# Optimization experiments

Hardware: AMD Instinct MI355X
Metric: run time of the kernel (lower is better)

Reference implementation:

```python
import jax, jax.numpy as jnp
import numpy as np

B, C, H, W = 8, 512, 64, 64
CH = C // 2          # channels per branch after chunk
R = CH // 4          # reduced channels (reduction=4)


def conv1x1(x, w, b):
    # x: [B,c,H,W], w: [o,c], b: [o]  (1x1 conv == per-pixel matmul)
    return jnp.einsum('oc,bchw->bohw', w, x) + b[None, :, None, None]


def spatial_self_corr(x, w1, b1, w2, b2, wo, bo):
    # DANet-style position attention. x: [B,CH,H,W]
    b_, c_, h_, w_ = x.shape
    n = h_ * w_
    q = conv1x1(x, w1, b1).reshape(b_, -1, n)   # [B,R,N]
    k = conv1x1(x, w2, b2).reshape(b_, -1, n)   # [B,R,N]
    attn = jax.nn.softmax(jnp.einsum('brn,brm->bnm', q, k), axis=-1)  # [B,N,N]
    out = jnp.einsum('brn,bnm->brm', k, attn)   # v = k (reduced channels), [B,R,N]
    out = out.reshape(b_, -1, h_, w_)
    return conv1x1(out, wo, bo)                 # [B,CH,H,W]


def channel_self_corr(x, wq, bq, wk, bk, wo, bo):
    # DANet-style channel attention over reduced channels. x: [B,CH,H,W]
    b_, c_, h_, w_ = x.shape
    n = h_ * w_
    q = conv1x1(x, wq, bq).reshape(b_, -1, n)   # [B,R,N]
    k = conv1x1(x, wk, bk).reshape(b_, -1, n)   # [B,R,N]
    attn = jax.nn.softmax(jnp.einsum('brn,bsn->brs', q, k), axis=-1)  # [B,R,R]
    out = jnp.einsum('brs,bsn->brn', attn, k)   # v = k (reduced channels)
    out = out.reshape(b_, -1, h_, w_)
    return conv1x1(out, wo, bo)                 # [B,CH,H,W]


def ckam_forward(top_feat, bottom_feat, wt, bt, wb, bb,
                 s_w1, s_b1, s_w2, s_b2, s_wo, s_bo,
                 c_wq, c_bq, c_wk, c_bk, c_wo, c_bo, f_w, f_b):
    top = conv1x1(top_feat, wt, bt)
    bottom = conv1x1(bottom_feat, wb, bb)
    x = top + bottom                            # [B,C,H,W]
    x1, x2 = jnp.split(x, 2, axis=1)            # each [B,C/2,H,W]
    ssc_out = spatial_self_corr(x1, s_w1, s_b1, s_w2, s_b2, s_wo, s_bo)
    csc_out = channel_self_corr(x2, c_wq, c_bq, c_wk, c_bk, c_wo, c_bo)
    out = jnp.concatenate([ssc_out, csc_out], axis=1)  # [B,C,H,W]
    return conv1x1(out, f_w, f_b)


def setup_inputs() -> dict:
    key = jax.random.key(0)
    ks = jax.random.split(key, 24)
    s = 0.02
    d = {
        'top_feat': jax.random.normal(ks[0], (B, C, H, W), jnp.float32),
        'bottom_feat': jax.random.normal(ks[1], (B, C, H, W), jnp.float32),
        'wt': jax.random.normal(ks[2], (C, C), jnp.float32) * s,
        'bt': jnp.zeros((C,), jnp.float32),
        'wb': jax.random.normal(ks[3], (C, C), jnp.float32) * s,
        'bb': jnp.zeros((C,), jnp.float32),
        's_w1': jax.random.normal(ks[4], (R, CH), jnp.float32) * s,
        's_b1': jnp.zeros((R,), jnp.float32),
        's_w2': jax.random.normal(ks[5], (R, CH), jnp.float32) * s,
        's_b2': jnp.zeros((R,), jnp.float32),
        's_wo': jax.random.normal(ks[6], (CH, R), jnp.float32) * s,
        's_bo': jnp.zeros((CH,), jnp.float32),
        'c_wq': jax.random.normal(ks[7], (R, CH), jnp.float32) * s,
        'c_bq': jnp.zeros((R,), jnp.float32),
        'c_wk': jax.random.normal(ks[8], (R, CH), jnp.float32) * s,
        'c_bk': jnp.zeros((R,), jnp.float32),
        'c_wo': jax.random.normal(ks[9], (CH, R), jnp.float32) * s,
        'c_bo': jnp.zeros((CH,), jnp.float32),
        'f_w': jax.random.normal(ks[10], (C, C), jnp.float32) * s,
        'f_b': jnp.zeros((C,), jnp.float32),
    }
    return d


def reference(top_feat, bottom_feat, wt, bt, wb, bb,
              s_w1, s_b1, s_w2, s_b2, s_wo, s_bo,
              c_wq, c_bq, c_wk, c_bk, c_wo, c_bo, f_w, f_b):
    return ckam_forward(top_feat, bottom_feat, wt, bt, wb, bb,
                        s_w1, s_b1, s_w2, s_b2, s_wo, s_bo,
                        c_wq, c_bq, c_wk, c_bk, c_wo, c_bo, f_w, f_b)
```

## Files before the change

kernel.cpp:

```cpp
#include <hip/hip_runtime.h>

typedef unsigned short u16;
typedef unsigned int   u32;
typedef __attribute__((ext_vector_type(8))) short short8;
typedef __attribute__((ext_vector_type(4))) float f32x4;

__device__ __forceinline__ u16 f2bf(float f) {
  u32 u = __float_as_uint(f);
  u32 r = u + 0x7fffu + ((u >> 16) & 1u);
  return (u16)(r >> 16);
}

__device__ __forceinline__ void gl_lds16(const u16* g, u16* l) {
  __builtin_amdgcn_global_load_lds(
      (const __attribute__((address_space(1))) u32*)g,
      (__attribute__((address_space(3))) u32*)l, 16, 0, 0);
}

__global__ __launch_bounds__(256) void k_combine_qk(
    const float* __restrict__ wt, const float* __restrict__ bt,
    const float* __restrict__ wb, const float* __restrict__ bb,
    const float* __restrict__ s_w1, const float* __restrict__ s_b1,
    const float* __restrict__ s_w2, const float* __restrict__ s_b2,
    const float* __restrict__ c_wq, const float* __restrict__ c_bq,
    const float* __restrict__ c_wk, const float* __restrict__ c_bk,
    u16* __restrict__ Wqkb, float* __restrict__ bqk) {
  int j = blockIdx.x;
  int g = j >> 6, r = j & 63;
  const float* sw; const float* sb;
  if (g == 0)      { sw = s_w1; sb = s_b1; }
  else if (g == 1) { sw = s_w2; sb = s_b2; }
  else if (g == 2) { sw = c_wq; sb = c_bq; }
  else             { sw = c_wk; sb = c_bk; }
  int cbase = (g < 2) ? 0 : 256;

  __shared__ float swr[256];
  __shared__ float red[256];
  int t = threadIdx.x;
  swr[t] = sw[r * 256 + t];
  __syncthreads();

  float a0 = 0.f, a1 = 0.f, a2 = 0.f, a3 = 0.f;
#pragma unroll 4
  for (int c = 0; c < 256; ++c) {
    float a = swr[c];
    int row = (cbase + c) * 512;
    a0 += a * wt[row + t];
    a1 += a * wt[row + 256 + t];
    a2 += a * wb[row + t];
    a3 += a * wb[row + 256 + t];
  }
  Wqkb[j * 1024 + t]       = f2bf(a0);
  Wqkb[j * 1024 + 256 + t] = f2bf(a1);
  Wqkb[j * 1024 + 512 + t] = f2bf(a2);
  Wqkb[j * 1024 + 768 + t] = f2bf(a3);

  red[t] = swr[t] * (bt[cbase + t] + bb[cbase + t]);
  __syncthreads();
  for (int s = 128; s > 0; s >>= 1) {
    if (t < s) red[t] += red[t + s];
    __syncthreads();
  }
  if (t == 0) bqk[j] = red[0] + sb[r];
}

__global__ __launch_bounds__(128) void k_combine_f(
    const float* __restrict__ f_w, const float* __restrict__ f_b,
    const float* __restrict__ s_wo, const float* __restrict__ s_bo,
    const float* __restrict__ c_wo, const float* __restrict__ c_bo,
    u16* __restrict__ Wfb, float* __restrict__ bfb) {
  int o = blockIdx.x;
  int t = threadIdx.x;
  __shared__ float fwr[512];
  __shared__ float red[128];
  for (int i = t; i < 512; i += 128) fwr[i] = f_w[o * 512 + i];
  __syncthreads();

  float acc = 0.f;
  if (t < 64) {
#pragma unroll 4
    for (int c = 0; c < 256; ++c) acc += fwr[c] * s_wo[c * 64 + t];
  } else {
    int rr = t - 64;
#pragma unroll 4
    for (int c = 0; c < 256; ++c) acc += fwr[256 + c] * c_wo[c * 64 + rr];
  }
  Wfb[o * 128 + t] = f2bf(acc);

  red[t] = fwr[t] * s_bo[t] + fwr[t + 128] * s_bo[t + 128]
         + fwr[256 + t] * c_bo[t] + fwr[384 + t] * c_bo[t + 128];
  __syncthreads();
  for (int s = 64; s > 0; s >>= 1) {
    if (t < s) red[t] += red[t + s];
    __syncthreads();
  }
  if (t == 0) bfb[o] = red[0] + f_b[o];
}

__global__ __launch_bounds__(256) void k_gemm_qk_mfma(
    const float* __restrict__ top, const float* __restrict__ bot,
    const u16* __restrict__ Wqkb, const float* __restrict__ bqk,
    float* __restrict__ qk) {
  int b = blockIdx.z, j0 = blockIdx.y * 128, n0 = blockIdx.x * 128;
  __shared__ __align__(16) u16 Aj[2][128][32];
  __shared__ __align__(16) u16 Xs[2][128][32];
  int t = threadIdx.x;
  int wv = t >> 6, lane = t & 63;
  int wr = wv >> 1, wc = wv & 1;
  int q = lane >> 4, l = lane & 15;

  f32x4 acc[4][4];
#pragma unroll
  for (int tr = 0; tr < 4; ++tr)
#pragma unroll
    for (int tc = 0; tc < 4; ++tc) acc[tr][tc] = (f32x4){0.f, 0.f, 0.f, 0.f};

  int xn = t & 31;
  int xs = t >> 5;
  int kx = (xn + (xn >> 2)) & 3;
  int wcol = ((((xs >> 1) ^ kx) << 4) | ((xs & 1) << 3));
  int asr4 = lane >> 2;
  int asc = (lane & 3) ^ ((asr4 + (asr4 >> 2)) & 3);
  int rowA = wr * 64 + l;
  int rowX = wc * 64 + l;
  int fswA = (q ^ ((rowA + (rowA >> 2)) & 3)) << 4;
  int fswX = (q ^ ((rowX + (rowX >> 2)) & 3)) << 4;

  float xva[16], xvb[16];

  auto stageA = [&](int kc, u16* dst) {
#pragma unroll
    for (int pp = 0; pp < 2; ++pp) {
      int p = wv * 2 + pp;
      int row = p * 16 + asr4;
      gl_lds16(Wqkb + (size_t)(j0 + row) * 1024 + kc + asc * 8, dst + p * 512);
    }
  };
  auto loadX = [&](int kc, float (&xv)[16]) {
    const float* src = (kc < 512) ? top : bot;
    int c0 = kc & 511;
    const float* xb = src + (size_t)(b * 512 + c0) * 4096 + n0;
#pragma unroll
    for (int p = 0; p < 4; ++p) {
      int n = xn + 32 * p;
#pragma unroll
      for (int d = 0; d < 4; ++d)
        xv[4 * p + d] = xb[(size_t)(4 * xs + d) * 4096 + n];
    }
  };
  auto writeX = [&](float (&xv)[16], u16* dst) {
    char* base = reinterpret_cast<char*>(dst);
#pragma unroll
    for (int p = 0; p < 4; ++p) {
      int n = xn + 32 * p;
      uint2 pk;
      pk.x = (u32)f2bf(xv[4 * p])     | ((u32)f2bf(xv[4 * p + 1]) << 16);
      pk.y = (u32)f2bf(xv[4 * p + 2]) | ((u32)f2bf(xv[4 * p + 3]) << 16);
      *reinterpret_cast<uint2*>(base + n * 64 + wcol) = pk;
    }
  };
  auto compute = [&](int bufsel) {
    const char* Ab = reinterpret_cast<const char*>(&Aj[bufsel][0][0]);
    const char* Xb = reinterpret_cast<const char*>(&Xs[bufsel][0][0]);
    short8 af[4], bfr[4];
#pragma unroll
    for (int tr = 0; tr < 4; ++tr)
      af[tr] = *reinterpret_cast<const short8*>(Ab + (rowA + tr * 16) * 64 + fswA);
#pragma unroll
    for (int tc = 0; tc < 4; ++tc)
      bfr[tc] = *reinterpret_cast<const short8*>(Xb + (rowX + tc * 16) * 64 + fswX);
#pragma unroll
    for (int tr = 0; tr < 4; ++tr)
#pragma unroll
      for (int tc = 0; tc < 4; ++tc)
        acc[tr][tc] = __builtin_amdgcn_mfma_f32_16x16x32_bf16(
            af[tr], bfr[tc], acc[tr][tc], 0, 0, 0);
  };

  stageA(0, &Aj[0][0][0]);
  loadX(0, xva);
  writeX(xva, &Xs[0][0][0]);
  loadX(32, xvb);
  asm volatile("s_waitcnt lgkmcnt(0)" ::: "memory");
  __builtin_amdgcn_s_barrier();

  for (int it2 = 0; it2 < 15; ++it2) {
    int e = it2 * 2;
    stageA((e + 1) * 32, &Aj[1][0][0]);
    loadX((e + 2) * 32, xva);
    writeX(xvb, &Xs[1][0][0]);
    compute(0);
    asm volatile("s_waitcnt vmcnt(16) lgkmcnt(0)" ::: "memory");
    __builtin_amdgcn_s_barrier();
    stageA((e + 2) * 32, &Aj[0][0][0]);
    loadX((e + 3) * 32, xvb);
    writeX(xva, &Xs[0][0][0]);
    compute(1);
    asm volatile("s_waitcnt vmcnt(16) lgkmcnt(0)" ::: "memory");
    __builtin_amdgcn_s_barrier();
  }
  stageA(31 * 32, &Aj[1][0][0]);
  writeX(xvb, &Xs[1][0][0]);
  compute(0);
  asm volatile("s_waitcnt vmcnt(0) lgkmcnt(0)" ::: "memory");
  __builtin_amdgcn_s_barrier();
  compute(1);

#pragma unroll
  for (int tr = 0; tr < 4; ++tr) {
    int j = j0 + wr * 64 + tr * 16 + q * 4;
    float4 bias = *reinterpret_cast<const float4*>(&bqk[j]);
#pragma unroll
    for (int tc = 0; tc < 4; ++tc) {
      int n = n0 + wc * 64 + tc * 16 + l;
      float* dst = qk + (size_t)(b * 256 + j) * 4096 + n;
      dst[0]        = acc[tr][tc][0] + bias.x;
      dst[4096]     = acc[tr][tc][1] + bias.y;
      dst[2 * 4096] = acc[tr][tc][2] + bias.z;
      dst[3 * 4096] = acc[tr][tc][3] + bias.w;
    }
  }
}

__global__ __launch_bounds__(256) void k_transpose_qk(
    const float* __restrict__ qk, u16* __restrict__ q1t, u16* __restrict__ k1t) {
  int b = blockIdx.y, n0 = blockIdx.x * 64;
  __shared__ u16 T[128][68];
  int t = threadIdx.x;
  for (int i = t; i < 8192; i += 256) {
    int j = i >> 6, n = i & 63;
    T[j][n] = f2bf(qk[((size_t)(b * 256) + j) * 4096 + n0 + n]);
  }
  __syncthreads();
  int n = t & 63, h = t >> 6;
  u16 buf[32];
#pragma unroll
  for (int jj = 0; jj < 32; ++jj) buf[jj] = T[h * 32 + jj][n];
  u16* dst;
  if (h < 2) dst = q1t + ((size_t)(b * 4096) + n0 + n) * 64 + h * 32;
  else       dst = k1t + ((size_t)(b * 4096) + n0 + n) * 64 + (h - 2) * 32;
  u32* d32 = reinterpret_cast<u32*>(dst);
#pragma unroll
  for (int k = 0; k < 16; ++k)
    d32[k] = (u32)buf[2 * k] | ((u32)buf[2 * k + 1] << 16);
}

__global__ __launch_bounds__(256) void k_sp_stats_mfma(
    const u16* __restrict__ q1t, const u16* __restrict__ k1t,
    const float* __restrict__ qk, u16* __restrict__ k1d) {
  int b = blockIdx.y, n0 = blockIdx.x * 64;
  __shared__ u16 Qs[64][72];
  __shared__ float red[4][64][16];
  __shared__ float dvs[64];
  int t = threadIdx.x;
  int wv = t >> 6, lane = t & 63;
  int q = lane >> 4, l = lane & 15;

  {
    const u32* src = reinterpret_cast<const u32*>(q1t + ((size_t)(b * 4096) + n0) * 64);
    for (int i = t; i < 2048; i += 256) {
      int n = i >> 5, c = i & 31;
      reinterpret_cast<u32*>(&Qs[n][0])[c] = src[n * 32 + c];
    }
  }
  __syncthreads();

  short8 afr[4][2];
#pragma unroll
  for (int tn = 0; tn < 4; ++tn)
#pragma unroll
    for (int kh = 0; kh < 2; ++kh)
      afr[tn][kh] = *reinterpret_cast<const short8*>(&Qs[tn * 16 + l][kh * 32 + q * 8]);

  const u16* kbase = k1t + (size_t)b * 4096 * 64;
  float dsum[4][4];
#pragma unroll
  for (int tn = 0; tn < 4; ++tn)
#pragma unroll
    for (int i = 0; i < 4; ++i) dsum[tn][i] = 0.f;

  for (int mt = wv; mt < 64; mt += 4) {
    int m0 = mt * 64;
#pragma unroll
    for (int tm = 0; tm < 4; ++tm) {
      const u16* kp = kbase + ((size_t)(m0 + tm * 16 + l)) * 64;
      short8 b0 = *reinterpret_cast<const short8*>(kp + q * 8);
      short8 b1 = *reinterpret_cast<const short8*>(kp + 32 + q * 8);
#pragma unroll
      for (int tn = 0; tn < 4; ++tn) {
        f32x4 acc = {0.f, 0.f, 0.f, 0.f};
        acc = __builtin_amdgcn_mfma_f32_16x16x32_bf16(afr[tn][0], b0, acc, 0, 0, 0);
        acc = __builtin_amdgcn_mfma_f32_16x16x32_bf16(afr[tn][1], b1, acc, 0, 0, 0);
#pragma unroll
        for (int i = 0; i < 4; ++i) dsum[tn][i] += __expf(acc[i]);
      }
    }
  }

#pragma unroll
  for (int tn = 0; tn < 4; ++tn)
#pragma unroll
    for (int i = 0; i < 4; ++i)
      red[wv][tn * 16 + q * 4 + i][l] = dsum[tn][i];
  __syncthreads();
  if (t < 64) {
    float s = 0.f;
#pragma unroll
    for (int v = 0; v < 4; ++v)
#pragma unroll
      for (int u = 0; u < 16; ++u) s += red[v][t][u];
    dvs[t] = 1.0f / s;
  }
  __syncthreads();

  const float* k1src = qk + ((size_t)(b * 256) + 64) * 4096 + n0;
  u16* kdst = k1d + (size_t)(b * 64) * 4096 + n0;
  for (int i = t; i < 4096; i += 256) {
    int r = i >> 6, n = i & 63;
    kdst[(size_t)r * 4096 + n] = f2bf(k1src[(size_t)r * 4096 + n] * dvs[n]);
  }
}

#define NSPLIT 2

__device__ __forceinline__ void stage_qk(const u16* qb, const u16* kb, int noff,
                                         u16* qdst, u16* kdst,
                                         int wv, int rsub, int scol) {
#pragma unroll
  for (int pp = 0; pp < 2; ++pp) {
    int p = wv * 2 + pp;
    int row = p * 8 + rsub;
    gl_lds16(qb + ((size_t)(noff + row)) * 64 + scol * 8, qdst + p * 512);
    gl_lds16(kb + (size_t)row * 4096 + noff + scol * 8, kdst + p * 512);
  }
}

__global__ __launch_bounds__(256) void k_sp_apply_mfma(
    const u16* __restrict__ q1t, const u16* __restrict__ k1t,
    const u16* __restrict__ k1d, float* __restrict__ spre) {
  int b = blockIdx.z, m0 = blockIdx.x * 64;
  int n_base = blockIdx.y * (4096 / NSPLIT);
  const int NT = 64 / NSPLIT;

  __shared__ __align__(16) u16 Qs[2][64][64];
  __shared__ __align__(16) u16 Ks[2][64][64];
  __shared__ __align__(16) u16 Wt[64][64];

  int t = threadIdx.x;
  int wv = t >> 6, lane = t & 63;
  int q = lane >> 4, l = lane & 15;
  int sw = l & 7;
  int rsub = lane >> 3;
  int scol = (lane & 7) ^ rsub;

  const u16* ktp = k1t + ((size_t)(b * 4096) + m0 + wv * 16 + l) * 64;
  short8 bS0 = *reinterpret_cast<const short8*>(ktp + q * 8);
  short8 bS1 = *reinterpret_cast<const short8*>(ktp + 32 + q * 8);

  const u16* qb = q1t + (size_t)b * 4096 * 64;
  const u16* kb = k1d + (size_t)b * 64 * 4096;

  f32x4 accO[4];
#pragma unroll
  for (int tr = 0; tr < 4; ++tr) accO[tr] = (f32x4){0.f, 0.f, 0.f, 0.f};

  stage_qk(qb, kb, n_base, &Qs[0][0][0], &Ks[0][0][0], wv, rsub, scol);
  __syncthreads();

  int wrow = wv * 16 + l;
  char* wp = reinterpret_cast<char*>(&Wt[wrow][0]);
  int c_a0 = (q ^ sw) << 4;
  int c_a1 = c_a0 ^ 64;

  int cur = 0;
  for (int nt = 0; nt < NT; ++nt) {
    if (nt + 1 < NT)
      stage_qk(qb, kb, n_base + (nt + 1) * 64,
               &Qs[cur ^ 1][0][0], &Ks[cur ^ 1][0][0], wv, rsub, scol);

    const u16(*Qc)[64] = Qs[cur];
    const u16(*Kc)[64] = Ks[cur];

#pragma unroll
    for (int tn = 0; tn < 4; ++tn) {
      const char* qrow = reinterpret_cast<const char*>(&Qc[tn * 16 + l][0]);
      short8 a0 = *reinterpret_cast<const short8*>(qrow + c_a0);
      short8 a1 = *reinterpret_cast<const short8*>(qrow + c_a1);
      f32x4 s = {0.f, 0.f, 0.f, 0.f};
      s = __builtin_amdgcn_mfma_f32_16x16x32_bf16(a0, bS0, s, 0, 0, 0);
      s = __builtin_amdgcn_mfma_f32_16x16x32_bf16(a1, bS1, s, 0, 0, 0);
      u16 w0 = f2bf(__expf(s[0]));
      u16 w1 = f2bf(__expf(s[1]));
      u16 w2 = f2bf(__expf(s[2]));
      u16 w3 = f2bf(__expf(s[3]));
      uint2 pk;
      pk.x = (u32)w0 | ((u32)w1 << 16);
      pk.y = (u32)w2 | ((u32)w3 << 16);
      *reinterpret_cast<uint2*>(
          wp + ((((tn * 2 + (q >> 1)) ^ sw) << 4) | ((q & 1) << 3))) = pk;
    }

    short8 bW0 = *reinterpret_cast<const short8*>(wp + c_a0);
    short8 bW1 = *reinterpret_cast<const short8*>(wp + c_a1);
#pragma unroll
    for (int tr = 0; tr < 4; ++tr) {
      const char* krow = reinterpret_cast<const char*>(&Kc[tr * 16 + l][0]);
      short8 a0 = *reinterpret_cast<const short8*>(krow + c_a0);
      short8 a1 = *reinterpret_cast<const short8*>(krow + c_a1);
      accO[tr] = __builtin_amdgcn_mfma_f32_16x16x32_bf16(a0, bW0, accO[tr], 0, 0, 0);
      accO[tr] = __builtin_amdgcn_mfma_f32_16x16x32_bf16(a1, bW1, accO[tr], 0, 0, 0);
    }

    __syncthreads();
    cur ^= 1;
  }

#pragma unroll
  for (int tr = 0; tr < 4; ++tr)
#pragma unroll
    for (int i = 0; i < 4; ++i)
      atomicAdd(&spre[(size_t)(b * 64 + tr * 16 + q * 4 + i) * 4096 + m0 + wrow],
                accO[tr][i]);
}

__global__ __launch_bounds__(256) void k_ch_scores(
    const float* __restrict__ qk, float* __restrict__ part) {
  int b = blockIdx.y, ch = blockIdx.x;
  const float* q2 = qk + (size_t)(b * 256 + 128) * 4096;
  const float* k2 = qk + (size_t)(b * 256 + 192) * 4096;
  __shared__ float Qs[64][65];
  __shared__ float Ks[64][65];
  int t = threadIdx.x, ti = t >> 4, tj = t & 15;
  float acc[4][4] = {};

  for (int sub = 0; sub < 2; ++sub) {
    int n0 = ch * 128 + sub * 64;
    __syncthreads();
    for (int i = t; i < 4096; i += 256) {
      int r = i >> 6, n = i & 63;
      Qs[r][n] = q2[(size_t)r * 4096 + n0 + n];
      Ks[r][n] = k2[(size_t)r * 4096 + n0 + n];
    }
    __syncthreads();
#pragma unroll
    for (int n = 0; n < 64; ++n) {
      float qa[4], ka[4];
#pragma unroll
      for (int i = 0; i < 4; ++i) qa[i] = Qs[ti * 4 + i][n];
#pragma unroll
      for (int jx = 0; jx < 4; ++jx) ka[jx] = Ks[tj * 4 + jx][n];
#pragma unroll
      for (int i = 0; i < 4; ++i)
#pragma unroll
        for (int jx = 0; jx < 4; ++jx) acc[i][jx] += qa[i] * ka[jx];
    }
  }
#pragma unroll
  for (int i = 0; i < 4; ++i)
#pragma unroll
    for (int jx = 0; jx < 4; ++jx)
      part[(size_t)(b * 32 + ch) * 4096 + (ti * 4 + i) * 64 + tj * 4 + jx] = acc[i][jx];
}

__global__ __launch_bounds__(64) void k_ch_softmax(
    const float* __restrict__ part, float* __restrict__ attn2) {
  int bid = blockIdx.x;
  int b = bid >> 6, r = bid & 63;
  int s = threadIdx.x;
  const float* p0 = part + (size_t)(b * 32) * 4096 + r * 64 + s;
  float sum = 0.f;
#pragma unroll
  for (int c = 0; c < 32; ++c) sum += p0[(size_t)c * 4096];
  float mx = sum;
#pragma unroll
  for (int o = 32; o > 0; o >>= 1) mx = fmaxf(mx, __shfl_xor(mx, o));
  float e = __expf(sum - mx);
  float den = e;
#pragma unroll
  for (int o = 32; o > 0; o >>= 1) den += __shfl_xor(den, o);
  attn2[(size_t)b * 4096 + r * 64 + s] = e / den;
}

__global__ __launch_bounds__(256) void k_ch_apply(
    const float* __restrict__ qk, const float* __restrict__ attn2,
    float* __restrict__ cpre) {
  int b = blockIdx.y;
  int t = threadIdx.x;
  int n = blockIdx.x * 64 + (t & 63);
  int qr = t >> 6;
  const float* k2 = qk + (size_t)(b * 256 + 192) * 4096;
  __shared__ float As[64][64];
  {
    float4* As4 = reinterpret_cast<float4*>(&As[0][0]);
    const float4* a4 = reinterpret_cast<const float4*>(attn2 + (size_t)b * 4096);
    for (int i = t; i < 1024; i += 256) As4[i] = a4[i];
  }
  __syncthreads();

  float acc[16];
#pragma unroll
  for (int rr = 0; rr < 16; ++rr) acc[rr] = 0.f;
  for (int s4 = 0; s4 < 64; s4 += 4) {
    float kv0 = k2[(size_t)(s4 + 0) * 4096 + n];
    float kv1 = k2[(size_t)(s4 + 1) * 4096 + n];
    float kv2 = k2[(size_t)(s4 + 2) * 4096 + n];
    float kv3 = k2[(size_t)(s4 + 3) * 4096 + n];
#pragma unroll
    for (int rr = 0; rr < 16; ++rr) {
      float4 w = *reinterpret_cast<const float4*>(&As[qr * 16 + rr][s4]);
      acc[rr] += w.x * kv0 + w.y * kv1 + w.z * kv2 + w.w * kv3;
    }
  }
#pragma unroll
  for (int rr = 0; rr < 16; ++rr)
    cpre[(size_t)(b * 64 + qr * 16 + rr) * 4096 + n] = acc[rr];
}

__global__ __launch_bounds__(256) void k_final_mfma(
    const float* __restrict__ spre, const float* __restrict__ cpre,
    const u16* __restrict__ Wfb, const float* __restrict__ bfb,
    float* __restrict__ out) {
  int b = blockIdx.z, o0 = blockIdx.y * 128, n0 = blockIdx.x * 128;
  __shared__ u16 Aj[128][40];
  __shared__ u16 Xs[128][40];
  int t = threadIdx.x;
  int wv = t >> 6, lane = t & 63;
  int wr = wv >> 1, wc = wv & 1;
  int q = lane >> 4, l = lane & 15;

  f32x4 acc[4][4];
#pragma unroll
  for (int tr = 0; tr < 4; ++tr)
#pragma unroll
    for (int tc = 0; tc < 4; ++tc) acc[tr][tc] = (f32x4){0.f, 0.f, 0.f, 0.f};

  int xn = t & 31;
  int xs = t >> 5;

  for (int kc = 0; kc < 128; kc += 32) {
    __syncthreads();
    {
      const u32* asrc = reinterpret_cast<const u32*>(Wfb + (size_t)o0 * 128 + kc);
#pragma unroll
      for (int p = 0; p < 8; ++p) {
        int i = p * 256 + t;
        int row = i >> 4, c = i & 15;
        *reinterpret_cast<u32*>(&Aj[row][c * 2]) = asrc[(size_t)row * 64 + c];
      }
    }
    const float* src = (kc < 64) ? spre : cpre;
    int r0 = (kc < 64) ? kc : kc - 64;
    const float* xb = src + (size_t)(b * 64 + r0) * 4096 + n0;
#pragma unroll
    for (int p = 0; p < 8; ++p) {
      int n = xn + 32 * (p >> 1);
      int kp = xs + 8 * (p & 1);
      float v0 = xb[(size_t)(2 * kp) * 4096 + n];
      float v1 = xb[(size_t)(2 * kp + 1) * 4096 + n];
      *reinterpret_cast<u32*>(&Xs[n][kp * 2]) =
          (u32)f2bf(v0) | ((u32)f2bf(v1) << 16);
    }
    __syncthreads();

    short8 af[4], bfr[4];
#pragma unroll
    for (int tr = 0; tr < 4; ++tr)
      af[tr] = *reinterpret_cast<const short8*>(&Aj[wr * 64 + tr * 16 + l][q * 8]);
#pragma unroll
    for (int tc = 0; tc < 4; ++tc)
      bfr[tc] = *reinterpret_cast<const short8*>(&Xs[wc * 64 + tc * 16 + l][q * 8]);
#pragma unroll
    for (int tr = 0; tr < 4; ++tr)
#pragma unroll
      for (int tc = 0; tc < 4; ++tc)
        acc[tr][tc] = __builtin_amdgcn_mfma_f32_16x16x32_bf16(
            af[tr], bfr[tc], acc[tr][tc], 0, 0, 0);
  }

#pragma unroll
  for (int tr = 0; tr < 4; ++tr) {
    int o = o0 + wr * 64 + tr * 16 + q * 4;
    float4 bias = *reinterpret_cast<const float4*>(&bfb[o]);
#pragma unroll
    for (int tc = 0; tc < 4; ++tc) {
      int n = n0 + wc * 64 + tc * 16 + l;
      float* dst = out + (size_t)(b * 512 + o) * 4096 + n;
      dst[0]        = acc[tr][tc][0] + bias.x;
      dst[4096]     = acc[tr][tc][1] + bias.y;
      dst[2 * 4096] = acc[tr][tc][2] + bias.z;
      dst[3 * 4096] = acc[tr][tc][3] + bias.w;
    }
  }
}

extern "C" void kernel_launch(void* const* d_in, const int* in_sizes, int n_in,
                              void* d_out, int out_size, void* d_ws, size_t ws_size,
                              hipStream_t stream) {
  const float* top  = (const float*)d_in[0];
  const float* bot  = (const float*)d_in[1];
  const float* wt   = (const float*)d_in[2];
  const float* bt   = (const float*)d_in[3];
  const float* wb   = (const float*)d_in[4];
  const float* bb   = (const float*)d_in[5];
  const float* s_w1 = (const float*)d_in[6];
  const float* s_b1 = (const float*)d_in[7];
  const float* s_w2 = (const float*)d_in[8];
  const float* s_b2 = (const float*)d_in[9];
  const float* s_wo = (const float*)d_in[10];
  const float* s_bo = (const float*)d_in[11];
  const float* c_wq = (const float*)d_in[12];
  const float* c_bq = (const float*)d_in[13];
  const float* c_wk = (const float*)d_in[14];
  const float* c_bk = (const float*)d_in[15];
  const float* c_wo = (const float*)d_in[16];
  const float* c_bo = (const float*)d_in[17];
  const float* f_w  = (const float*)d_in[18];
  const float* f_b  = (const float*)d_in[19];
  float* out = (float*)d_out;

  char* ob = (char*)d_out;
  float* qk = (float*)ob;
  u16* q1t = (u16*)(ob + 33554432);
  u16* k1t = (u16*)(ob + 37748736);
  u16* k1d = (u16*)(ob + 41943040);
  float* part = (float*)(ob + 46137344);

  char* ws = (char*)d_ws;
  float* attn2 = (float*)(ws + 1179648);
  float* spre  = (float*)(ws + 1310720);
  float* cpre  = (float*)(ws + 9699328);
  u16*   Wqkb  = (u16*)  (ws + 18087936);
  float* bqk   = (float*)(ws + 18612224);
  u16*   Wfb   = (u16*)  (ws + 18613248);
  float* bfb   = (float*)(ws + 18744320);

  hipMemsetAsync(spre, 0, 8388608, stream);

  k_combine_qk<<<256, 256, 0, stream>>>(wt, bt, wb, bb, s_w1, s_b1, s_w2, s_b2,
                                        c_wq, c_bq, c_wk, c_bk, Wqkb, bqk);
  k_combine_f<<<512, 128, 0, stream>>>(f_w, f_b, s_wo, s_bo, c_wo, c_bo, Wfb, bfb);
  k_gemm_qk_mfma<<<dim3(32, 2, 8), 256, 0, stream>>>(top, bot, Wqkb, bqk, qk);
  k_transpose_qk<<<dim3(64, 8), 256, 0, stream>>>(qk, q1t, k1t);
  k_sp_stats_mfma<<<dim3(64, 8), 256, 0, stream>>>(q1t, k1t, qk, k1d);
  k_ch_scores<<<dim3(32, 8), 256, 0, stream>>>(qk, part);
  k_ch_softmax<<<512, 64, 0, stream>>>(part, attn2);
  k_ch_apply<<<dim3(64, 8), 256, 0, stream>>>(qk, attn2, cpre);
  k_sp_apply_mfma<<<dim3(64, NSPLIT, 8), 256, 0, stream>>>(q1t, k1t, k1d, spre);
  k_final_mfma<<<dim3(32, 4, 8), 256, 0, stream>>>(spre, cpre, Wfb, bfb, out);
}
```

Baseline: 433.2 us.

## Vectorize fp32 activation loads and double-buffer the final GEMM

The QK projection GEMM now loads activations as float4 vectors, with each thread covering four adjacent pixels, and the vmcnt waits are adjusted to match the smaller number of load instructions. The transpose kernel drops its LDS staging and reads float4 rows directly, packing bf16 into 16-byte stores. The final 1x1 GEMM is rebuilt on the same double-buffered, swizzled LDS pipeline, with async global-to-LDS weight staging. The aim is fewer memory instructions and better overlap of loads with MFMA work. The risk is that the uint2 LDS writes may hit more bank conflicts.

```diff
diff --git a/kernel.cpp b/kernel.cpp
--- a/kernel.cpp
+++ b/kernel.cpp
@@ -115,10 +115,8 @@
 #pragma unroll
     for (int tc = 0; tc < 4; ++tc) acc[tr][tc] = (f32x4){0.f, 0.f, 0.f, 0.f};
 
-  int xn = t & 31;
+  int a = t & 31;
   int xs = t >> 5;
-  int kx = (xn + (xn >> 2)) & 3;
-  int wcol = ((((xs >> 1) ^ kx) << 4) | ((xs & 1) << 3));
   int asr4 = lane >> 2;
   int asc = (lane & 3) ^ ((asr4 + (asr4 >> 2)) & 3);
   int rowA = wr * 64 + l;
@@ -126,7 +124,7 @@
   int fswA = (q ^ ((rowA + (rowA >> 2)) & 3)) << 4;
   int fswX = (q ^ ((rowX + (rowX >> 2)) & 3)) << 4;
 
-  float xva[16], xvb[16];
+  f32x4 xva[4], xvb[4];
 
   auto stageA = [&](int kc, u16* dst) {
 #pragma unroll
@@ -136,27 +134,25 @@
       gl_lds16(Wqkb + (size_t)(j0 + row) * 1024 + kc + asc * 8, dst + p * 512);
     }
   };
-  auto loadX = [&](int kc, float (&xv)[16]) {
+  auto loadX = [&](int kc, f32x4 (&xv)[4]) {
     const float* src = (kc < 512) ? top : bot;
     int c0 = kc & 511;
-    const float* xb = src + (size_t)(b * 512 + c0) * 4096 + n0;
-#pragma unroll
-    for (int p = 0; p < 4; ++p) {
-      int n = xn + 32 * p;
-#pragma unroll
-      for (int d = 0; d < 4; ++d)
-        xv[4 * p + d] = xb[(size_t)(4 * xs + d) * 4096 + n];
-    }
-  };
-  auto writeX = [&](float (&xv)[16], u16* dst) {
+    const float* xb = src + (size_t)(b * 512 + c0) * 4096 + n0 + 4 * a;
+#pragma unroll
+    for (int d = 0; d < 4; ++d)
+      xv[d] = *reinterpret_cast<const f32x4*>(&xb[(size_t)(4 * xs + d) * 4096]);
+  };
+  auto writeX = [&](f32x4 (&xv)[4], u16* dst) {
     char* base = reinterpret_cast<char*>(dst);
 #pragma unroll
-    for (int p = 0; p < 4; ++p) {
-      int n = xn + 32 * p;
+    for (int i = 0; i < 4; ++i) {
+      int n = 4 * a + i;
+      int key = (n + (n >> 2)) & 3;
+      int col = ((((xs >> 1) ^ key) << 4) | ((xs & 1) << 3));
       uint2 pk;
-      pk.x = (u32)f2bf(xv[4 * p])     | ((u32)f2bf(xv[4 * p + 1]) << 16);
-      pk.y = (u32)f2bf(xv[4 * p + 2]) | ((u32)f2bf(xv[4 * p + 3]) << 16);
-      *reinterpret_cast<uint2*>(base + n * 64 + wcol) = pk;
+      pk.x = (u32)f2bf(xv[0][i]) | ((u32)f2bf(xv[1][i]) << 16);
+      pk.y = (u32)f2bf(xv[2][i]) | ((u32)f2bf(xv[3][i]) << 16);
+      *reinterpret_cast<uint2*>(base + n * 64 + col) = pk;
     }
   };
   auto compute = [&](int bufsel) {
@@ -190,13 +186,13 @@
     loadX((e + 2) * 32, xva);
     writeX(xvb, &Xs[1][0][0]);
     compute(0);
-    asm volatile("s_waitcnt vmcnt(16) lgkmcnt(0)" ::: "memory");
+    asm volatile("s_waitcnt vmcnt(4) lgkmcnt(0)" ::: "memory");
     __builtin_amdgcn_s_barrier();
     stageA((e + 2) * 32, &Aj[0][0][0]);
     loadX((e + 3) * 32, xvb);
     writeX(xva, &Xs[0][0][0]);
     compute(1);
-    asm volatile("s_waitcnt vmcnt(16) lgkmcnt(0)" ::: "memory");
+    asm volatile("s_waitcnt vmcnt(4) lgkmcnt(0)" ::: "memory");
     __builtin_amdgcn_s_barrier();
   }
   stageA(31 * 32, &Aj[1][0][0]);
@@ -225,24 +221,27 @@
 __global__ __launch_bounds__(256) void k_transpose_qk(
     const float* __restrict__ qk, u16* __restrict__ q1t, u16* __restrict__ k1t) {
   int b = blockIdx.y, n0 = blockIdx.x * 64;
-  __shared__ u16 T[128][68];
-  int t = threadIdx.x;
-  for (int i = t; i < 8192; i += 256) {
-    int j = i >> 6, n = i & 63;
-    T[j][n] = f2bf(qk[((size_t)(b * 256) + j) * 4096 + n0 + n]);
-  }
-  __syncthreads();
-  int n = t & 63, h = t >> 6;
-  u16 buf[32];
-#pragma unroll
-  for (int jj = 0; jj < 32; ++jj) buf[jj] = T[h * 32 + jj][n];
-  u16* dst;
-  if (h < 2) dst = q1t + ((size_t)(b * 4096) + n0 + n) * 64 + h * 32;
-  else       dst = k1t + ((size_t)(b * 4096) + n0 + n) * 64 + (h - 2) * 32;
-  u32* d32 = reinterpret_cast<u32*>(dst);
-#pragma unroll
-  for (int k = 0; k < 16; ++k)
-    d32[k] = (u32)buf[2 * k] | ((u32)buf[2 * k + 1] << 16);
+  int t = threadIdx.x;
+  int a = t & 15;
+  int c = t >> 4;
+  int jb = 8 * (c & 7);
+  const float* src =
+      qk + ((size_t)(b * 256) + (c >> 3) * 64 + jb) * 4096 + n0 + 4 * a;
+  f32x4 v[8];
+#pragma unroll
+  for (int i = 0; i < 8; ++i)
+    v[i] = *reinterpret_cast<const f32x4*>(&src[(size_t)i * 4096]);
+  u16* dstbase = (c < 8) ? q1t : k1t;
+#pragma unroll
+  for (int i = 0; i < 4; ++i) {
+    int n = n0 + 4 * a + i;
+    u32 pk[4];
+#pragma unroll
+    for (int kk = 0; kk < 4; ++kk)
+      pk[kk] = (u32)f2bf(v[2 * kk][i]) | ((u32)f2bf(v[2 * kk + 1][i]) << 16);
+    *reinterpret_cast<uint4*>(dstbase + ((size_t)(b * 4096) + n) * 64 + jb) =
+        *reinterpret_cast<const uint4*>(pk);
+  }
 }
 
 __global__ __launch_bounds__(256) void k_sp_stats_mfma(
@@ -521,8 +520,8 @@
     const u16* __restrict__ Wfb, const float* __restrict__ bfb,
     float* __restrict__ out) {
   int b = blockIdx.z, o0 = blockIdx.y * 128, n0 = blockIdx.x * 128;
-  __shared__ u16 Aj[128][40];
-  __shared__ u16 Xs[128][40];
+  __shared__ __align__(16) u16 Aj[2][128][32];
+  __shared__ __align__(16) u16 Xs[2][128][32];
   int t = threadIdx.x;
   int wv = t >> 6, lane = t & 63;
   int wr = wv >> 1, wc = wv & 1;
@@ -534,48 +533,88 @@
 #pragma unroll
     for (int tc = 0; tc < 4; ++tc) acc[tr][tc] = (f32x4){0.f, 0.f, 0.f, 0.f};
 
-  int xn = t & 31;
+  int a = t & 31;
   int xs = t >> 5;
-
-  for (int kc = 0; kc < 128; kc += 32) {
-    __syncthreads();
-    {
-      const u32* asrc = reinterpret_cast<const u32*>(Wfb + (size_t)o0 * 128 + kc);
-#pragma unroll
-      for (int p = 0; p < 8; ++p) {
-        int i = p * 256 + t;
-        int row = i >> 4, c = i & 15;
-        *reinterpret_cast<u32*>(&Aj[row][c * 2]) = asrc[(size_t)row * 64 + c];
-      }
-    }
+  int asr4 = lane >> 2;
+  int asc = (lane & 3) ^ ((asr4 + (asr4 >> 2)) & 3);
+  int rowA = wr * 64 + l;
+  int rowX = wc * 64 + l;
+  int fswA = (q ^ ((rowA + (rowA >> 2)) & 3)) << 4;
+  int fswX = (q ^ ((rowX + (rowX >> 2)) & 3)) << 4;
+
+  f32x4 xva[4], xvb[4];
+
+  auto stageA = [&](int kc, u16* dst) {
+#pragma unroll
+    for (int pp = 0; pp < 2; ++pp) {
+      int p = wv * 2 + pp;
+      int row = p * 16 + asr4;
+      gl_lds16(Wfb + (size_t)(o0 + row) * 128 + kc + asc * 8, dst + p * 512);
+    }
+  };
+  auto loadX = [&](int kc, f32x4 (&xv)[4]) {
     const float* src = (kc < 64) ? spre : cpre;
-    int r0 = (kc < 64) ? kc : kc - 64;
-    const float* xb = src + (size_t)(b * 64 + r0) * 4096 + n0;
-#pragma unroll
-    for (int p = 0; p < 8; ++p) {
-      int n = xn + 32 * (p >> 1);
-      int kp = xs + 8 * (p & 1);
-      float v0 = xb[(size_t)(2 * kp) * 4096 + n];
-      float v1 = xb[(size_t)(2 * kp + 1) * 4096 + n];
-      *reinterpret_cast<u32*>(&Xs[n][kp * 2]) =
-          (u32)f2bf(v0) | ((u32)f2bf(v1) << 16);
-    }
-    __syncthreads();
-
+    int r0 = kc & 63;
+    const float* xb = src + (size_t)(b * 64 + r0) * 4096 + n0 + 4 * a;
+#pragma unroll
+    for (int d = 0; d < 4; ++d)
+      xv[d] = *reinterpret_cast<const f32x4*>(&xb[(size_t)(4 * xs + d) * 4096]);
+  };
+  auto writeX = [&](f32x4 (&xv)[4], u16* dst) {
+    char* base = reinterpret_cast<char*>(dst);
+#pragma unroll
+    for (int i = 0; i < 4; ++i) {
+      int n = 4 * a + i;
+      int key = (n + (n >> 2)) & 3;
+      int col = ((((xs >> 1) ^ key) << 4) | ((xs & 1) << 3));
+      uint2 pk;
+      pk.x = (u32)f2bf(xv[0][i]) | ((u32)f2bf(xv[1][i]) << 16);
+      pk.y = (u32)f2bf(xv[2][i]) | ((u32)f2bf(xv[3][i]) << 16);
+      *reinterpret_cast<uint2*>(base + n * 64 + col) = pk;
+    }
+  };
+  auto compute = [&](int bufsel) {
+    const char* Ab = reinterpret_cast<const char*>(&Aj[bufsel][0][0]);
+    const char* Xb = reinterpret_cast<const char*>(&Xs[bufsel][0][0]);
     short8 af[4], bfr[4];
 #pragma unroll
     for (int tr = 0; tr < 4; ++tr)
-      af[tr] = *reinterpret_cast<const short8*>(&Aj[wr * 64 + tr * 16 + l][q * 8]);
+      af[tr] = *reinterpret_cast<const short8*>(Ab + (rowA + tr * 16) * 64 + fswA);
 #pragma unroll
     for (int tc = 0; tc < 4; ++tc)
-      bfr[tc] = *reinterpret_cast<const short8*>(&Xs[wc * 64 + tc * 16 + l][q * 8]);
+      bfr[tc] = *reinterpret_cast<const short8*>(Xb + (rowX + tc * 16) * 64 + fswX);
 #pragma unroll
     for (int tr = 0; tr < 4; ++tr)
 #pragma unroll
       for (int tc = 0; tc < 4; ++tc)
         acc[tr][tc] = __builtin_amdgcn_mfma_f32_16x16x32_bf16(
             af[tr], bfr[tc], acc[tr][tc], 0, 0, 0);
-  }
+  };
+
+  stageA(0, &Aj[0][0][0]);
+  loadX(0, xva);
+  writeX(xva, &Xs[0][0][0]);
+  loadX(32, xvb);
+  asm volatile("s_waitcnt lgkmcnt(0)" ::: "memory");
+  __builtin_amdgcn_s_barrier();
+  stageA(32, &Aj[1][0][0]);
+  loadX(64, xva);
+  writeX(xvb, &Xs[1][0][0]);
+  compute(0);
+  asm volatile("s_waitcnt vmcnt(4) lgkmcnt(0)" ::: "memory");
+  __builtin_amdgcn_s_barrier();
+  stageA(64, &Aj[0][0][0]);
+  loadX(96, xvb);
+  writeX(xva, &Xs[0][0][0]);
+  compute(1);
+  asm volatile("s_waitcnt vmcnt(4) lgkmcnt(0)" ::: "memory");
+  __builtin_amdgcn_s_barrier();
+  stageA(96, &Aj[1][0][0]);
+  writeX(xvb, &Xs[1][0][0]);
+  compute(0);
+  asm volatile("s_waitcnt vmcnt(0) lgkmcnt(0)" ::: "memory");
+  __builtin_amdgcn_s_barrier();
+  compute(1);
 
 #pragma unroll
   for (int tr = 0; tr < 4; ++tr) {
```

Result: no change. 433.6 us (+0.1%).
